# Performance work log

Measured on AMD Instinct MI355X. Metric: run time of the kernel, lower is better.

The kernel has to match this reference:

```python
import jax, jax.numpy as jnp
import numpy as np
from jax.scipy.special import erfinv

EMBED = 384
HEADS = 6
HEAD_DIM = EMBED // HEADS  # 64
N_FREQS = HEAD_DIM // 2    # 32
SEQ = 1025                 # 1 CLS + 32*32 patches
POS_DIM = 2
MIN_FREQ, MAX_FREQ = 0.1, 1000.0


def _phi(m: int) -> float:
    x = 2.0
    for _ in range(10):
        x = (1.0 + x) ** (1.0 / (m + 1.0))
    return x


def _uniform_directions(n: int, d: int) -> jnp.ndarray:
    # golden-ratio quasi-random directions, normalized (matches uniform_directions_jax)
    g = _phi(d)
    alpha = (1.0 / g) ** jnp.arange(1, d + 1, dtype=jnp.float32)
    i = jnp.arange(1, n + 1, dtype=jnp.float32)[:, None]
    z = jnp.fmod(i * alpha, 1.0)
    dirs = erfinv(2.0 * z - 1.0)
    return dirs / jnp.linalg.norm(dirs, axis=1, keepdims=True)


def _rope_freqs() -> jnp.ndarray:  # [h, F, P]
    omega = MIN_FREQ * (MAX_FREQ / MIN_FREQ) ** jnp.linspace(0.0, 1.0, N_FREQS)
    dirs = _uniform_directions(HEADS * N_FREQS, POS_DIM).reshape(HEADS, N_FREQS, POS_DIM)
    return dirs * omega.reshape(1, N_FREQS, 1)


def _coords_2d() -> jnp.ndarray:  # [S, 2], CLS at origin, patches in [-1,1]^2
    n = int(np.sqrt(SEQ - 1))  # 32
    yy, xx = jnp.meshgrid(jnp.arange(n), jnp.arange(n), indexing='ij')
    xf = xx.flatten().astype(jnp.float32) / (n - 1) * 2 - 1
    yf = yy.flatten().astype(jnp.float32) / (n - 1) * 2 - 1
    patch = jnp.stack([xf, yf], axis=1)
    return jnp.concatenate([jnp.zeros((1, 2), jnp.float32), patch], axis=0)


def _apply_rope(t_bshd, freqs_hFP, coords_SP):
    # theta: [S, h, F]
    theta = jnp.einsum('hfp,sp->shf', freqs_hFP, coords_SP)
    cos, sin = jnp.cos(theta), jnp.sin(theta)  # broadcast over batch
    x1, y1 = jnp.split(t_bshd, 2, axis=-1)     # [b,s,h,F] each
    return jnp.concatenate([x1 * cos - y1 * sin, x1 * sin + y1 * cos], axis=-1)


def setup_inputs() -> dict:
    key = jax.random.key(0)
    ks = jax.random.split(key, 6)
    scale = 1.0 / np.sqrt(EMBED)
    return {
        'x':  jax.random.normal(ks[0], (16, SEQ, EMBED), jnp.float32),
        'Wq': jax.random.normal(ks[1], (EMBED, EMBED), jnp.float32) * scale,
        'Wk': jax.random.normal(ks[2], (EMBED, EMBED), jnp.float32) * scale,
        'Wv': jax.random.normal(ks[3], (EMBED, EMBED), jnp.float32) * scale,
        'Wo': jax.random.normal(ks[4], (EMBED, EMBED), jnp.float32) * scale,
        'bo': jnp.zeros((EMBED,), jnp.float32),
    }


def reference(x, Wq, Wk, Wv, Wo, bo):
    b, s, e = x.shape
    freqs = _rope_freqs()   # constant buffers
    coords = _coords_2d()
    q = (x @ Wq).reshape(b, s, HEADS, HEAD_DIM)
    k = (x @ Wk).reshape(b, s, HEADS, HEAD_DIM)
    v = (x @ Wv).reshape(b, s, HEADS, HEAD_DIM)
    q = _apply_rope(q, freqs, coords)
    k = _apply_rope(k, freqs, coords)
    scores = jnp.einsum('blhd,bmhd->bhlm', q, k) / np.sqrt(HEAD_DIM)
    attn = jax.nn.softmax(scores, axis=-1)
    out = jnp.einsum('bhlm,bmhd->blhd', attn, v).reshape(b, s, e)
    return out @ Wo + bo
```

## Files before the change

### kernel.cpp

```cpp
#include <hip/hip_runtime.h>
#include <hip/hip_bf16.h>
#include <math.h>

#define EMBED 384
#define HEADS 6
#define HD    64
#define NF    32
#define SEQ   1025
#define SEQP  1088
#define BATCH 16
#define MTOT  (BATCH*SEQ)
#define NCHUNK 17
#define LSTRIDE 72
#define VSTR   68
#define GSTR 40
#define NHEAVY 768

typedef __bf16 bf16x8 __attribute__((ext_vector_type(8)));
typedef __bf16 bf16x4 __attribute__((ext_vector_type(4)));
typedef float  f32x4  __attribute__((ext_vector_type(4)));
typedef short  s16x4  __attribute__((ext_vector_type(4)));

#define MFMA_BF16(A,B,C) __builtin_amdgcn_mfma_f32_16x16x32_bf16((A),(B),(C),0,0,0)
#define MFMA16(A,B,C) __builtin_amdgcn_mfma_f32_16x16x16bf16_1k((A),(B),(C),0,0,0)

__device__ __forceinline__ __bf16 f2bf(float f){
    __hip_bfloat16 h = __float2bfloat16(f);
    return *reinterpret_cast<__bf16*>(&h);
}
__device__ __forceinline__ short bfbits(float f){
    __hip_bfloat16 h = __float2bfloat16(f);
    return *reinterpret_cast<short*>(&h);
}
__device__ __forceinline__ float bf2f(__bf16 b){
    unsigned short u = __builtin_bit_cast(unsigned short, b);
    unsigned int x = (unsigned int)u << 16;
    return __builtin_bit_cast(float, x);
}

__global__ __launch_bounds__(256) void x_to_bf16_kernel(
    const float* __restrict__ x, __hip_bfloat16* __restrict__ xb)
{
    const int n4 = MTOT*EMBED/4;
    int i = blockIdx.x*256 + threadIdx.x;
    if (i < n4){
        float4 v = *reinterpret_cast<const float4*>(x + (size_t)i*4);
        bf16x4 b; b[0]=f2bf(v.x); b[1]=f2bf(v.y); b[2]=f2bf(v.z); b[3]=f2bf(v.w);
        *reinterpret_cast<bf16x4*>(reinterpret_cast<__bf16*>(xb) + (size_t)i*4) = b;
    }
}

__global__ __launch_bounds__(256) void transpose_w_kernel(
    const float* __restrict__ Wq, const float* __restrict__ Wk,
    const float* __restrict__ Wv, const float* __restrict__ Wo,
    __hip_bfloat16* __restrict__ Wt)
{
    __shared__ float tile[64][65];
    const int mat = blockIdx.z;
    const float* W = (mat==0)?Wq:(mat==1)?Wk:(mat==2)?Wv:Wo;
    const int k0 = blockIdx.x*64, n0 = blockIdx.y*64;
    const int c = threadIdx.x & 63, rq = threadIdx.x >> 6;
    #pragma unroll
    for (int i = 0; i < 16; ++i){
        int row = rq*16 + i;
        tile[row][c] = W[(size_t)(k0+row)*EMBED + n0 + c];
    }
    __syncthreads();
    #pragma unroll
    for (int i = 0; i < 16; ++i){
        int nr = rq*16 + i;
        Wt[((size_t)mat*EMBED + n0 + nr)*EMBED + k0 + c] = __float2bfloat16(tile[c][nr]);
    }
}

__device__ __forceinline__ float erfinv_f(float x){
    float w = -log1pf(-x*x);
    float p;
    if (w < 5.0f){
        w -= 2.5f;
        p = 2.81022636e-08f;
        p = fmaf(p, w, 3.43273939e-07f);
        p = fmaf(p, w, -3.5233877e-06f);
        p = fmaf(p, w, -4.39150654e-06f);
        p = fmaf(p, w, 0.00021858087f);
        p = fmaf(p, w, -0.00125372503f);
        p = fmaf(p, w, -0.00417768164f);
        p = fmaf(p, w, 0.246640727f);
        p = fmaf(p, w, 1.50140941f);
    } else {
        w = sqrtf(w) - 3.0f;
        p = -0.000200214257f;
        p = fmaf(p, w, 0.000100950558f);
        p = fmaf(p, w, 0.00134934322f);
        p = fmaf(p, w, -0.00367342844f);
        p = fmaf(p, w, 0.00573950773f);
        p = fmaf(p, w, -0.0076224613f);
        p = fmaf(p, w, 0.00943887047f);
        p = fmaf(p, w, 1.00167406f);
        p = fmaf(p, w, 2.83297682f);
    }
    return p * x;
}

__global__ void rope_tables_kernel(float* __restrict__ cos_t, float* __restrict__ sin_t){
    int idx = blockIdx.x * blockDim.x + threadIdx.x;
    if (idx >= SEQ*HEADS*NF) return;
    int f  = idx & (NF-1);
    int hf = idx / NF;
    int h  = hf % HEADS;
    int s  = hf / HEADS;

    double xd = 2.0;
    #pragma unroll
    for (int it = 0; it < 10; ++it) xd = cbrt(1.0 + xd);
    float a1 = (float)(1.0 / xd);
    float a2 = a1 * a1;

    float fi = (float)(h*NF + f + 1);
    float z1 = fmodf(fi * a1, 1.0f);
    float z2 = fmodf(fi * a2, 1.0f);
    float d1 = erfinv_f(2.0f*z1 - 1.0f);
    float d2 = erfinv_f(2.0f*z2 - 1.0f);
    float inv = 1.0f / sqrtf(d1*d1 + d2*d2);
    d1 *= inv; d2 *= inv;

    float omega = 0.1f * powf(10000.0f, (float)f / 31.0f);
    float fx = d1 * omega, fy = d2 * omega;

    float cx = 0.0f, cy = 0.0f;
    if (s > 0){
        int pi = s - 1;
        cx = (float)(pi & 31) / 31.0f * 2.0f - 1.0f;
        cy = (float)(pi >> 5) / 31.0f * 2.0f - 1.0f;
    }
    float theta = fx*cx + fy*cy;
    float sv, cv;
    sincosf(theta, &sv, &cv);
    cos_t[idx] = cv;
    sin_t[idx] = sv;
}

__global__ __launch_bounds__(256, 3) void qkv_rope_kernel(
    const __hip_bfloat16* __restrict__ xb_,
    const __hip_bfloat16* __restrict__ Wt,
    const float* __restrict__ cos_t,
    const float* __restrict__ sin_t,
    __hip_bfloat16* __restrict__ qbuf,
    __hip_bfloat16* __restrict__ kbuf,
    __hip_bfloat16* __restrict__ vbuf)
{
    __shared__ __align__(16) __bf16 xs[128*GSTR];
    __shared__ __align__(16) __bf16 bt[128*GSTR];
    const int tid = threadIdx.x;
    const int m0 = blockIdx.x * 128;
    const int j  = blockIdx.y;
    const __bf16* xb = reinterpret_cast<const __bf16*>(xb_);
    const __bf16* wt = reinterpret_cast<const __bf16*>(Wt);

    int soff[2], arow[2], brow[2];
    #pragma unroll
    for (int i = 0; i < 2; ++i){
        int g = tid + i*256;
        int row = g >> 2, kc = g & 3;
        soff[i] = row*GSTR + kc*8;
        int am = m0 + row; if (am > MTOT-1) am = MTOT-1;
        arow[i] = am;
        brow[i] = j*128 + row;
    }

    bf16x8 ar[2], br[2];
    #pragma unroll
    for (int i = 0; i < 2; ++i){
        int g = tid + i*256, kc = g & 3;
        ar[i] = *reinterpret_cast<const bf16x8*>(xb + (size_t)arow[i]*EMBED + kc*8);
        br[i] = *reinterpret_cast<const bf16x8*>(wt + (size_t)brow[i]*EMBED + kc*8);
    }

    const int w = tid >> 6;
    const int lane = tid & 63;
    const int quad = lane >> 4, low = lane & 15;
    const int mh = w >> 1, nh = w & 1;
    const int mw0 = m0 + mh*64;

    f32x4 acc[4][4] = {};
    for (int kb = 0; kb < 12; ++kb){
        __syncthreads();
        #pragma unroll
        for (int i = 0; i < 2; ++i){
            *reinterpret_cast<bf16x8*>(&xs[soff[i]]) = ar[i];
            *reinterpret_cast<bf16x8*>(&bt[soff[i]]) = br[i];
        }
        __syncthreads();
        if (kb < 11){
            const int k1 = (kb+1)*32;
            #pragma unroll
            for (int i = 0; i < 2; ++i){
                int g = tid + i*256, kc = g & 3;
                ar[i] = *reinterpret_cast<const bf16x8*>(xb + (size_t)arow[i]*EMBED + k1 + kc*8);
                br[i] = *reinterpret_cast<const bf16x8*>(wt + (size_t)brow[i]*EMBED + k1 + kc*8);
            }
        }
        bf16x8 af[4], bfr[4];
        #pragma unroll
        for (int mt = 0; mt < 4; ++mt)
            af[mt] = *reinterpret_cast<const bf16x8*>(&xs[(mh*64 + mt*16 + low)*GSTR + quad*8]);
        #pragma unroll
        for (int t = 0; t < 4; ++t)
            bfr[t] = *reinterpret_cast<const bf16x8*>(&bt[(nh*64 + t*16 + low)*GSTR + quad*8]);
        #pragma unroll
        for (int t = 0; t < 4; ++t)
            #pragma unroll
            for (int mt = 0; mt < 4; ++mt)
                acc[mt][t] = MFMA_BF16(af[mt], bfr[t], acc[mt][t]);
    }

    const int n64 = j*2 + nh;
    const int mat = n64 / 6;
    const int h   = n64 % 6;

    if (mat == 2){
        #pragma unroll
        for (int mt = 0; mt < 4; ++mt)
            #pragma unroll
            for (int t = 0; t < 4; ++t)
                #pragma unroll
                for (int r = 0; r < 4; ++r){
                    int m = mw0 + mt*16 + quad*4 + r;
                    if (m < MTOT){
                        int b = m / SEQ, s = m % SEQ;
                        vbuf[((size_t)(b*HEADS + h)*SEQ + s)*HD + t*16 + low] = __float2bfloat16(acc[mt][t][r]);
                    }
                }
    } else {
        __hip_bfloat16* ob = (mat == 0) ? qbuf : kbuf;
        const float qs_ = (mat == 0) ? 0.125f*1.44269504088896340736f : 1.0f;
        #pragma unroll
        for (int mt = 0; mt < 4; ++mt)
            #pragma unroll
            for (int t = 0; t < 2; ++t)
                #pragma unroll
                for (int r = 0; r < 4; ++r){
                    int m = mw0 + mt*16 + quad*4 + r;
                    if (m < MTOT){
                        int b = m / SEQ, s = m % SEQ;
                        int f = t*16 + low;
                        float cv = cos_t[(s*HEADS + h)*NF + f];
                        float sv = sin_t[(s*HEADS + h)*NF + f];
                        float x1 = acc[mt][t][r];
                        float y1 = acc[mt][t+2][r];
                        size_t base = ((size_t)(b*HEADS + h)*SEQ + s)*HD;
                        ob[base + f]      = __float2bfloat16((x1*cv - y1*sv)*qs_);
                        ob[base + NF + f] = __float2bfloat16((x1*sv + y1*cv)*qs_);
                    }
                }
    }
}

__global__ __launch_bounds__(256) void vt_transpose_kernel(
    const __hip_bfloat16* __restrict__ v, __hip_bfloat16* __restrict__ vt)
{
    __shared__ __bf16 tileT[64*72];
    const int tid = threadIdx.x;
    const int bh = blockIdx.x;
    const int s0 = blockIdx.y * 64;
    const __bf16* vb = reinterpret_cast<const __bf16*>(v) + (size_t)bh*SEQ*HD;
    #pragma unroll
    for (int i = 0; i < 2; ++i){
        int ch = tid + i*256;
        int srow = ch >> 3, dg = ch & 7;
        int s = s0 + srow; if (s > SEQ-1) s = SEQ-1;
        bf16x8 val = *reinterpret_cast<const bf16x8*>(vb + (size_t)s*HD + dg*8);
        #pragma unroll
        for (int e = 0; e < 8; ++e)
            tileT[(dg*8 + e)*72 + srow] = val[e];
    }
    __syncthreads();
    __bf16* ot = reinterpret_cast<__bf16*>(vt) + (size_t)bh*HD*SEQP;
    #pragma unroll
    for (int i = 0; i < 2; ++i){
        int ch = tid + i*256;
        int d = ch >> 3, sg = ch & 7;
        bf16x8 val = *reinterpret_cast<const bf16x8*>(&tileT[d*72 + sg*8]);
        *reinterpret_cast<bf16x8*>(ot + (size_t)d*SEQP + s0 + sg*8) = val;
    }
}

__global__ __launch_bounds__(256, 4) void attn_kernel(
    const __hip_bfloat16* __restrict__ qbuf,
    const __hip_bfloat16* __restrict__ kbuf,
    const __hip_bfloat16* __restrict__ vtbuf,
    const __hip_bfloat16* __restrict__ vbuf,
    __hip_bfloat16* __restrict__ aout)
{
    __shared__ __align__(16) __bf16 kls[64*LSTRIDE];
    __shared__ __align__(16) __bf16 vls[64*VSTR];
    const int tid  = threadIdx.x;
    const int w    = tid >> 6;
    const int lane = tid & 63;
    const int id = blockIdx.x;

    if (id >= NHEAVY){
        const int bh = id - NHEAVY;
        const int b = bh / HEADS, h = bh % HEADS;
        const __bf16* qr = reinterpret_cast<const __bf16*>(qbuf) + ((size_t)bh*SEQ + 1024)*HD;
        const __bf16* kb = reinterpret_cast<const __bf16*>(kbuf) + (size_t)bh*SEQ*HD;
        const __bf16* vb = reinterpret_cast<const __bf16*>(vbuf) + (size_t)bh*SEQ*HD;
        float* pbuf = reinterpret_cast<float*>(kls);
        float* lred = pbuf + 1056;
        float* ored = reinterpret_cast<float*>(vls);
        float lsum = 0.f;
        for (int k = tid; k < SEQ; k += 256){
            float s = 0.f;
            #pragma unroll
            for (int dg = 0; dg < 8; ++dg){
                bf16x8 k8 = *reinterpret_cast<const bf16x8*>(kb + (size_t)k*HD + dg*8);
                bf16x8 q8 = *reinterpret_cast<const bf16x8*>(qr + dg*8);
                #pragma unroll
                for (int e = 0; e < 8; ++e)
                    s = fmaf(bf2f(q8[e]), bf2f(k8[e]), s);
            }
            float p = exp2f(s);
            pbuf[k] = p;
            lsum += p;
        }
        #pragma unroll
        for (int off = 32; off; off >>= 1) lsum += __shfl_xor(lsum, off, 64);
        if (lane == 0) lred[w] = lsum;
        __syncthreads();
        const float ltot = lred[0] + lred[1] + lred[2] + lred[3];
        const int kbeg = w*256;
        const int kend = (w == 3) ? SEQ : kbeg + 256;
        float osum = 0.f;
        #pragma unroll 4
        for (int k = kbeg; k < kend; ++k)
            osum = fmaf(pbuf[k], bf2f(vb[(size_t)k*HD + lane]), osum);
        ored[w*64 + lane] = osum;
        __syncthreads();
        if (tid < 64){
            float o = ored[tid] + ored[64+tid] + ored[128+tid] + ored[192+tid];
            aout[((size_t)b*SEQ + 1024)*EMBED + h*HD + tid] = __float2bfloat16(o / ltot);
        }
        return;
    }

    const int quad = lane >> 4, low = lane & 15;
    const int bh = id % 96;
    const int qt = id / 96;
    const int b = bh / HEADS, h = bh % HEADS;
    const __bf16* qb = reinterpret_cast<const __bf16*>(qbuf);
    const __bf16* kb = reinterpret_cast<const __bf16*>(kbuf);
    const __bf16* vt = reinterpret_cast<const __bf16*>(vtbuf);
    const size_t base   = (size_t)bh * SEQ * HD;
    const size_t vtbase = (size_t)bh * HD * SEQP;
    const int q0 = qt*128 + w*32;

    int srow[2], sgk[2], soffk[2], soffv[2];
    #pragma unroll
    for (int i = 0; i < 2; ++i){
        int ch = tid + i*256;
        srow[i] = ch >> 3; sgk[i] = ch & 7;
        soffk[i] = srow[i]*LSTRIDE + sgk[i]*8;
        soffv[i] = srow[i]*VSTR    + sgk[i]*8;
    }

    bf16x8 bq[2][2];
    #pragma unroll
    for (int nt = 0; nt < 2; ++nt){
        int qs = q0 + nt*16 + low;
        #pragma unroll
        for (int ks = 0; ks < 2; ++ks)
            bq[nt][ks] = *reinterpret_cast<const bf16x8*>(qb + base + (size_t)qs*HD + ks*32 + quad*8);
    }

    bf16x8 kr[2], vr[2];
    #pragma unroll
    for (int i = 0; i < 2; ++i){
        int kk = srow[i]; if (kk > SEQ-1) kk = SEQ-1;
        kr[i] = *reinterpret_cast<const bf16x8*>(kb + base + (size_t)kk*HD + sgk[i]*8);
        vr[i] = *reinterpret_cast<const bf16x8*>(vt + vtbase + (size_t)srow[i]*SEQP + sgk[i]*8);
    }

    f32x4 o[2][4] = {};
    float l_i[2] = {0.f, 0.f};

    for (int c = 0; c < NCHUNK; ++c){
        const int c0 = c*64;
        __syncthreads();
        #pragma unroll
        for (int i = 0; i < 2; ++i){
            *reinterpret_cast<bf16x8*>(&kls[soffk[i]]) = kr[i];
            bf16x4 vlo = __builtin_shufflevector(vr[i], vr[i], 0,1,2,3);
            bf16x4 vhi = __builtin_shufflevector(vr[i], vr[i], 4,5,6,7);
            *reinterpret_cast<bf16x4*>(&vls[soffv[i]])     = vlo;
            *reinterpret_cast<bf16x4*>(&vls[soffv[i] + 4]) = vhi;
        }
        __syncthreads();
        if (c + 1 < NCHUNK){
            const int c1 = c0 + 64;
            #pragma unroll
            for (int i = 0; i < 2; ++i){
                int kk = c1 + srow[i]; if (kk > SEQ-1) kk = SEQ-1;
                kr[i] = *reinterpret_cast<const bf16x8*>(kb + base + (size_t)kk*HD + sgk[i]*8);
                vr[i] = *reinterpret_cast<const bf16x8*>(vt + vtbase + (size_t)srow[i]*SEQP + c1 + sgk[i]*8);
            }
        }
        f32x4 st[4][2] = {};
        #pragma unroll
        for (int kt = 0; kt < 4; ++kt)
            #pragma unroll
            for (int ks = 0; ks < 2; ++ks){
                bf16x8 ak = *reinterpret_cast<const bf16x8*>(&kls[(kt*16 + low)*LSTRIDE + ks*32 + quad*8]);
                #pragma unroll
                for (int nt = 0; nt < 2; ++nt)
                    st[kt][nt] = MFMA_BF16(ak, bq[nt][ks], st[kt][nt]);
            }
        if (c0 + 64 > SEQ){
            #pragma unroll
            for (int kt = 0; kt < 4; ++kt)
                #pragma unroll
                for (int r = 0; r < 4; ++r){
                    int key = c0 + kt*16 + quad*4 + r;
                    if (key >= SEQ){ st[kt][0][r] = -1e30f; st[kt][1][r] = -1e30f; }
                }
        }
        s16x4 pa[4][2];
        #pragma unroll
        for (int nt = 0; nt < 2; ++nt)
            #pragma unroll
            for (int kt = 0; kt < 4; ++kt)
                #pragma unroll
                for (int r = 0; r < 4; ++r){
                    float p = exp2f(st[kt][nt][r]);
                    l_i[nt] += p;
                    pa[kt][nt][r] = bfbits(p);
                }
        #pragma unroll
        for (int kt = 0; kt < 4; ++kt)
            #pragma unroll
            for (int dt = 0; dt < 4; ++dt){
                const s16x4 bv = *reinterpret_cast<const s16x4*>(&vls[(dt*16 + low)*VSTR + kt*16 + quad*4]);
                #pragma unroll
                for (int nt = 0; nt < 2; ++nt)
                    o[nt][dt] = MFMA16(pa[kt][nt], bv, o[nt][dt]);
            }
    }

    #pragma unroll
    for (int nt = 0; nt < 2; ++nt){
        l_i[nt] += __shfl_xor(l_i[nt], 16, 64);
        l_i[nt] += __shfl_xor(l_i[nt], 32, 64);
    }
    float lq[2][4];
    #pragma unroll
    for (int nt = 0; nt < 2; ++nt)
        #pragma unroll
        for (int r = 0; r < 4; ++r)
            lq[nt][r] = __shfl(l_i[nt], quad*4 + r, 64);

    #pragma unroll
    for (int nt = 0; nt < 2; ++nt)
        #pragma unroll
        for (int r = 0; r < 4; ++r){
            int s = q0 + nt*16 + quad*4 + r;
            float inv = 1.0f / lq[nt][r];
            __hip_bfloat16* dst = aout + ((size_t)b*SEQ + s)*EMBED + h*HD;
            #pragma unroll
            for (int dt = 0; dt < 4; ++dt)
                dst[dt*16 + low] = __float2bfloat16(o[nt][dt][r]*inv);
        }
}

__global__ __launch_bounds__(256, 3) void outproj_kernel(
    const __hip_bfloat16* __restrict__ a,
    const __hip_bfloat16* __restrict__ Wt,
    const float* __restrict__ bo,
    float* __restrict__ out)
{
    __shared__ __align__(16) __bf16 xs[128*GSTR];
    __shared__ __align__(16) __bf16 bt[128*GSTR];
    const int tid = threadIdx.x;
    const int m0 = blockIdx.x * 128;
    const int j  = blockIdx.y;
    const __bf16* ab = reinterpret_cast<const __bf16*>(a);
    const __bf16* wt = reinterpret_cast<const __bf16*>(Wt) + (size_t)3*EMBED*EMBED;

    int soff[2], arow[2], brow[2];
    #pragma unroll
    for (int i = 0; i < 2; ++i){
        int g = tid + i*256;
        int row = g >> 2, kc = g & 3;
        soff[i] = row*GSTR + kc*8;
        int am = m0 + row; if (am > MTOT-1) am = MTOT-1;
        arow[i] = am;
        brow[i] = j*128 + row;
    }
    bf16x8 ar[2], br[2];
    #pragma unroll
    for (int i = 0; i < 2; ++i){
        int g = tid + i*256, kc = g & 3;
        ar[i] = *reinterpret_cast<const bf16x8*>(ab + (size_t)arow[i]*EMBED + kc*8);
        br[i] = *reinterpret_cast<const bf16x8*>(wt + (size_t)brow[i]*EMBED + kc*8);
    }

    const int w = tid >> 6;
    const int lane = tid & 63;
    const int quad = lane >> 4, low = lane & 15;
    const int mh = w >> 1, nh = w & 1;
    const int mw0 = m0 + mh*64;
    const int n0 = j*128 + nh*64;

    f32x4 acc[4][4] = {};
    for (int kb = 0; kb < 12; ++kb){
        __syncthreads();
        #pragma unroll
        for (int i = 0; i < 2; ++i){
            *reinterpret_cast<bf16x8*>(&xs[soff[i]]) = ar[i];
            *reinterpret_cast<bf16x8*>(&bt[soff[i]]) = br[i];
        }
        __syncthreads();
        if (kb < 11){
            const int k1 = (kb+1)*32;
            #pragma unroll
            for (int i = 0; i < 2; ++i){
                int g = tid + i*256, kc = g & 3;
                ar[i] = *reinterpret_cast<const bf16x8*>(ab + (size_t)arow[i]*EMBED + k1 + kc*8);
                br[i] = *reinterpret_cast<const bf16x8*>(wt + (size_t)brow[i]*EMBED + k1 + kc*8);
            }
        }
        bf16x8 af[4], bfr[4];
        #pragma unroll
        for (int mt = 0; mt < 4; ++mt)
            af[mt] = *reinterpret_cast<const bf16x8*>(&xs[(mh*64 + mt*16 + low)*GSTR + quad*8]);
        #pragma unroll
        for (int t = 0; t < 4; ++t)
            bfr[t] = *reinterpret_cast<const bf16x8*>(&bt[(nh*64 + t*16 + low)*GSTR + quad*8]);
        #pragma unroll
        for (int t = 0; t < 4; ++t)
            #pragma unroll
            for (int mt = 0; mt < 4; ++mt)
                acc[mt][t] = MFMA_BF16(af[mt], bfr[t], acc[mt][t]);
    }

    #pragma unroll
    for (int t = 0; t < 4; ++t){
        const int n = n0 + t*16 + low;
        const float bias = bo[n];
        #pragma unroll
        for (int mt = 0; mt < 4; ++mt)
            #pragma unroll
            for (int r = 0; r < 4; ++r){
                const int m = mw0 + mt*16 + quad*4 + r;
                if (m < MTOT) out[(size_t)m*EMBED + n] = acc[mt][t][r] + bias;
            }
    }
}

extern "C" void kernel_launch(void* const* d_in, const int* in_sizes, int n_in,
                              void* d_out, int out_size, void* d_ws, size_t ws_size,
                              hipStream_t stream)
{
    const float* x  = (const float*)d_in[0];
    const float* Wq = (const float*)d_in[1];
    const float* Wk = (const float*)d_in[2];
    const float* Wv = (const float*)d_in[3];
    const float* Wo = (const float*)d_in[4];
    const float* bo = (const float*)d_in[5];
    float* out = (float*)d_out;

    const size_t NE = (size_t)MTOT * EMBED;
    const size_t VT = (size_t)BATCH*HEADS*HD*SEQP;
    char* ws = (char*)d_ws;
    size_t off = 0;
    __hip_bfloat16* qbuf = (__hip_bfloat16*)(ws + off); off += 2*NE;
    __hip_bfloat16* kbuf = (__hip_bfloat16*)(ws + off); off += 2*NE;
    __hip_bfloat16* abuf = (__hip_bfloat16*)(ws + off); off += 2*NE;
    __hip_bfloat16* vbuf = (__hip_bfloat16*)(ws + off); off += 2*NE;
    __hip_bfloat16* xbuf = (__hip_bfloat16*)(ws + off); off += 2*NE;
    __hip_bfloat16* vt   = (__hip_bfloat16*)(ws + off); off += 2*VT;
    __hip_bfloat16* Wt   = (__hip_bfloat16*)(ws + off); off += (size_t)4*EMBED*EMBED*2;
    float* cos_t = (float*)(ws + off); off += (size_t)SEQ*HEADS*NF*4;
    float* sin_t = (float*)(ws + off); off += (size_t)SEQ*HEADS*NF*4;

    x_to_bf16_kernel<<<dim3((MTOT*EMBED/4 + 255)/256), dim3(256), 0, stream>>>(x, xbuf);
    transpose_w_kernel<<<dim3(6,6,4), dim3(256), 0, stream>>>(Wq, Wk, Wv, Wo, Wt);
    rope_tables_kernel<<<dim3((SEQ*HEADS*NF + 255)/256), dim3(256), 0, stream>>>(cos_t, sin_t);
    qkv_rope_kernel<<<dim3((MTOT + 127)/128, 9), dim3(256), 0, stream>>>(xbuf, Wt, cos_t, sin_t, qbuf, kbuf, vbuf);
    vt_transpose_kernel<<<dim3(96, 17), dim3(256), 0, stream>>>(vbuf, vt);
    attn_kernel<<<dim3(NHEAVY + 96), dim3(256), 0, stream>>>(qbuf, kbuf, vt, vbuf, abuf);
    outproj_kernel<<<dim3((MTOT + 127)/128, 3), dim3(256), 0, stream>>>(abuf, Wt, bo, out);
}
```

Measured before the change: 208.0 us.

## Halve attention query tile per block and compute softmax row sums via MFMA

```diff
diff --git a/kernel.cpp b/kernel.cpp
--- a/kernel.cpp
+++ b/kernel.cpp
@@ -14,7 +14,7 @@
 #define LSTRIDE 72
 #define VSTR   68
 #define GSTR 40
-#define NHEAVY 768
+#define NHEAVY 1536
 
 typedef __bf16 bf16x8 __attribute__((ext_vector_type(8)));
 typedef __bf16 bf16x4 __attribute__((ext_vector_type(4)));
@@ -285,7 +285,7 @@
     }
 }
 
-__global__ __launch_bounds__(256, 4) void attn_kernel(
+__global__ __launch_bounds__(256, 6) void attn_kernel(
     const __hip_bfloat16* __restrict__ qbuf,
     const __hip_bfloat16* __restrict__ kbuf,
     const __hip_bfloat16* __restrict__ vtbuf,
@@ -352,7 +352,7 @@
     const __bf16* vt = reinterpret_cast<const __bf16*>(vtbuf);
     const size_t base   = (size_t)bh * SEQ * HD;
     const size_t vtbase = (size_t)bh * HD * SEQP;
-    const int q0 = qt*128 + w*32;
+    const int qw0 = qt*64 + w*16;
 
     int srow[2], sgk[2], soffk[2], soffv[2];
     #pragma unroll
@@ -363,13 +363,12 @@
         soffv[i] = srow[i]*VSTR    + sgk[i]*8;
     }
 
-    bf16x8 bq[2][2];
-    #pragma unroll
-    for (int nt = 0; nt < 2; ++nt){
-        int qs = q0 + nt*16 + low;
+    bf16x8 bq[2];
+    {
+        int qs = qw0 + low;
         #pragma unroll
         for (int ks = 0; ks < 2; ++ks)
-            bq[nt][ks] = *reinterpret_cast<const bf16x8*>(qb + base + (size_t)qs*HD + ks*32 + quad*8);
+            bq[ks] = *reinterpret_cast<const bf16x8*>(qb + base + (size_t)qs*HD + ks*32 + quad*8);
     }
 
     bf16x8 kr[2], vr[2];
@@ -380,8 +379,9 @@
         vr[i] = *reinterpret_cast<const bf16x8*>(vt + vtbase + (size_t)srow[i]*SEQP + sgk[i]*8);
     }
 
-    f32x4 o[2][4] = {};
-    float l_i[2] = {0.f, 0.f};
+    f32x4 o[4] = {};
+    f32x4 ol = {};
+    const s16x4 vone = {(short)0x3F80,(short)0x3F80,(short)0x3F80,(short)0x3F80};
 
     for (int c = 0; c < NCHUNK; ++c){
         const int c0 = c*64;
@@ -404,15 +404,13 @@
                 vr[i] = *reinterpret_cast<const bf16x8*>(vt + vtbase + (size_t)srow[i]*SEQP + c1 + sgk[i]*8);
             }
         }
-        f32x4 st[4][2] = {};
+        f32x4 st[4] = {};
         #pragma unroll
         for (int kt = 0; kt < 4; ++kt)
             #pragma unroll
             for (int ks = 0; ks < 2; ++ks){
                 bf16x8 ak = *reinterpret_cast<const bf16x8*>(&kls[(kt*16 + low)*LSTRIDE + ks*32 + quad*8]);
-                #pragma unroll
-                for (int nt = 0; nt < 2; ++nt)
-                    st[kt][nt] = MFMA_BF16(ak, bq[nt][ks], st[kt][nt]);
+                st[kt] = MFMA_BF16(ak, bq[ks], st[kt]);
             }
         if (c0 + 64 > SEQ){
             #pragma unroll
@@ -420,54 +418,35 @@
                 #pragma unroll
                 for (int r = 0; r < 4; ++r){
                     int key = c0 + kt*16 + quad*4 + r;
-                    if (key >= SEQ){ st[kt][0][r] = -1e30f; st[kt][1][r] = -1e30f; }
+                    if (key >= SEQ) st[kt][r] = -1e30f;
                 }
         }
-        s16x4 pa[4][2];
-        #pragma unroll
-        for (int nt = 0; nt < 2; ++nt)
-            #pragma unroll
-            for (int kt = 0; kt < 4; ++kt)
-                #pragma unroll
-                for (int r = 0; r < 4; ++r){
-                    float p = exp2f(st[kt][nt][r]);
-                    l_i[nt] += p;
-                    pa[kt][nt][r] = bfbits(p);
-                }
+        s16x4 pa[4];
         #pragma unroll
         for (int kt = 0; kt < 4; ++kt)
+            #pragma unroll
+            for (int r = 0; r < 4; ++r)
+                pa[kt][r] = bfbits(exp2f(st[kt][r]));
+        #pragma unroll
+        for (int kt = 0; kt < 4; ++kt){
+            ol = MFMA16(pa[kt], vone, ol);
             #pragma unroll
             for (int dt = 0; dt < 4; ++dt){
                 const s16x4 bv = *reinterpret_cast<const s16x4*>(&vls[(dt*16 + low)*VSTR + kt*16 + quad*4]);
-                #pragma unroll
-                for (int nt = 0; nt < 2; ++nt)
-                    o[nt][dt] = MFMA16(pa[kt][nt], bv, o[nt][dt]);
-            }
-    }
-
-    #pragma unroll
-    for (int nt = 0; nt < 2; ++nt){
-        l_i[nt] += __shfl_xor(l_i[nt], 16, 64);
-        l_i[nt] += __shfl_xor(l_i[nt], 32, 64);
-    }
-    float lq[2][4];
-    #pragma unroll
-    for (int nt = 0; nt < 2; ++nt)
-        #pragma unroll
-        for (int r = 0; r < 4; ++r)
-            lq[nt][r] = __shfl(l_i[nt], quad*4 + r, 64);
-
-    #pragma unroll
-    for (int nt = 0; nt < 2; ++nt)
-        #pragma unroll
-        for (int r = 0; r < 4; ++r){
-            int s = q0 + nt*16 + quad*4 + r;
-            float inv = 1.0f / lq[nt][r];
-            __hip_bfloat16* dst = aout + ((size_t)b*SEQ + s)*EMBED + h*HD;
-            #pragma unroll
-            for (int dt = 0; dt < 4; ++dt)
-                dst[dt*16 + low] = __float2bfloat16(o[nt][dt][r]*inv);
-        }
+                o[dt] = MFMA16(pa[kt], bv, o[dt]);
+            }
+        }
+    }
+
+    #pragma unroll
+    for (int r = 0; r < 4; ++r){
+        int s = qw0 + quad*4 + r;
+        float inv = 1.0f / ol[r];
+        __hip_bfloat16* dst = aout + ((size_t)b*SEQ + s)*EMBED + h*HD;
+        #pragma unroll
+        for (int dt = 0; dt < 4; ++dt)
+            dst[dt*16 + low] = __float2bfloat16(o[dt][r]*inv);
+    }
 }
 
 __global__ __launch_bounds__(256, 3) void outproj_kernel(
```

Result: slower. 217.7 us (+4.7%).
